# Kernel optimization log

Measured on AMD Instinct MI355X. Metric: run time of the kernel, lower is better.

The kernel has to match this reference:

```python
import jax, jax.numpy as jnp
import numpy as np

B, T, C = 8, 2048, 1024

def setup_inputs() -> dict:
    key = jax.random.key(0)
    ks = jax.random.split(key, 5)
    s_in = 1.0 / np.sqrt(C)
    s3 = 1.0 / np.sqrt(3 * C)
    return {
        'x': jax.random.normal(ks[0], (B, T, C), dtype=jnp.float32),
        'w_attn': jax.random.normal(ks[1], (C, 3 * C), dtype=jnp.float32) * s_in,
        'b_attn': jnp.zeros((3 * C,), dtype=jnp.float32),
        'w_proj': jax.random.normal(ks[2], (C, C), dtype=jnp.float32) * s_in,
        'b_proj': jnp.zeros((C,), dtype=jnp.float32),
    }

def reference(x, w_attn, b_attn, w_proj, b_proj):
    Bv, Tv, Cv = x.shape
    qkv = x @ w_attn + b_attn                      # [B,T,3C]
    q, k, v = jnp.split(qkv, 3, axis=-1)           # each [B,T,C]
    # causal additive mask, matching original -1e10 constant
    mask = jnp.where(jnp.tril(jnp.ones((Tv, Tv), dtype=jnp.bool_)), 0.0, -10000000000.0)
    attn = jnp.einsum('btc,bsc->bts', q, k) / jnp.sqrt(jnp.float32(Cv)) + mask
    attn = jax.nn.softmax(attn, axis=-1)           # [B,T,T]
    out = jnp.einsum('bts,bsc->btc', attn, v)      # [B,T,C]
    return out @ w_proj + b_proj
```

## Files before the change

kernel.cpp:

```cpp
#include <hip/hip_runtime.h>
#include <hip/hip_bf16.h>

typedef __hip_bfloat16 bf16_t;
typedef __attribute__((ext_vector_type(8))) __bf16 bf16x8;
typedef __attribute__((ext_vector_type(4))) float f32x4;
typedef __attribute__((ext_vector_type(8))) unsigned short u16x8;


__device__ __forceinline__ void gld_lds16(const void* g, void* l) {
    __builtin_amdgcn_global_load_lds(
        (const __attribute__((address_space(1))) unsigned int*)g,
        (__attribute__((address_space(3))) unsigned int*)l,
        16, 0, 0);
}

__device__ __forceinline__ unsigned short bf16_bits(float x) {
    bf16_t b = __float2bfloat16(x);
    return *reinterpret_cast<unsigned short*>(&b);
}


__global__ __launch_bounds__(256) void cvt_f32_bf16_kernel(
    const float* __restrict__ in, bf16_t* __restrict__ out, long n4) {
    long stride = (long)gridDim.x * blockDim.x;
    for (long i = (long)blockIdx.x * blockDim.x + threadIdx.x; i < n4; i += stride) {
        float4 v = reinterpret_cast<const float4*>(in)[i];
        ushort4 o;
        o.x = bf16_bits(v.x);
        o.y = bf16_bits(v.y);
        o.z = bf16_bits(v.z);
        o.w = bf16_bits(v.w);
        reinterpret_cast<ushort4*>(out)[i] = o;
    }
}


__global__ __launch_bounds__(256) void transpose_f32_bf16_kernel(
    const float* __restrict__ in, bf16_t* __restrict__ out, long ldin, long ldout) {
    __shared__ float tile[32][33];
    int c0 = blockIdx.x * 32, r0 = blockIdx.y * 32;
    int x = threadIdx.x;
#pragma unroll
    for (int yy = 0; yy < 4; ++yy) {
        int y = threadIdx.y + yy * 8;
        tile[y][x] = in[(long)(r0 + y) * ldin + c0 + x];
    }
    __syncthreads();
#pragma unroll
    for (int yy = 0; yy < 4; ++yy) {
        int y = threadIdx.y + yy * 8;
        out[(long)(c0 + y) * ldout + r0 + x] = __float2bfloat16(tile[x][y]);
    }
}

__global__ __launch_bounds__(256) void transpose_bf16_kernel(
    const bf16_t* __restrict__ in, bf16_t* __restrict__ out,
    long ldin, long ldout, long sIn, long sOut) {
    __shared__ bf16_t tile[32][33];
    in  += (long)blockIdx.z * sIn;
    out += (long)blockIdx.z * sOut;
    int c0 = blockIdx.x * 32, r0 = blockIdx.y * 32;
    int x = threadIdx.x;
#pragma unroll
    for (int yy = 0; yy < 4; ++yy) {
        int y = threadIdx.y + yy * 8;
        tile[y][x] = in[(long)(r0 + y) * ldin + c0 + x];
    }
    __syncthreads();
#pragma unroll
    for (int yy = 0; yy < 4; ++yy) {
        int y = threadIdx.y + yy * 8;
        out[(long)(c0 + y) * ldout + r0 + x] = tile[x][y];
    }
}


__global__ __launch_bounds__(512, 2) void gemm256_kernel(
    const bf16_t* __restrict__ A, const bf16_t* __restrict__ Bt,
    void* __restrict__ Cp, const float* __restrict__ bias,
    float scale, int K,
    long lda, long ldb, long ldc,
    long strideA, long strideB, long strideC,
    int mtiles, int causal_skip, int causal_klimit, int c_f32, int swz_mode)
{
    __shared__ __align__(16) bf16_t As[3][256 * 32];
    __shared__ __align__(16) bf16_t Bs[3][256 * 32];

    int nwg = gridDim.x;
    int bid = blockIdx.x;
    int bm_t, bn_t;
    if (swz_mode == 1 && (mtiles & 7) == 0 && (nwg & 7) == 0) {
        int xcd = bid & 7;
        int l   = bid >> 3;
        int mpx = mtiles >> 3;
        bm_t = xcd * mpx + (l % mpx);
        bn_t = l / mpx;
    } else {
        int swz = (bid & 7) * (nwg >> 3) + (bid >> 3);
        bm_t = swz % mtiles; bn_t = swz / mtiles;
    }
    if (causal_skip && bn_t > bm_t) return;
    long bm0 = (long)bm_t * 256, bn0 = (long)bn_t * 256;

    int b = blockIdx.z;
    const char* Ab = (const char*)(A + (long)b * strideA + bm0 * lda);
    const char* Bb = (const char*)(Bt + (long)b * strideB + bn0 * ldb);
    long ldab = lda * 2, ldbb = ldb * 2;

    int tid = threadIdx.x, wave = tid >> 6, lane = tid & 63;
    int wm = wave >> 2, wn = wave & 3;
    int lr = lane & 15, kc = lane >> 4;

    int Kend = K;
    if (causal_klimit) { long kl = bm0 + 256; Kend = (kl < (long)K) ? (int)kl : K; }
    int NT = Kend >> 5;

    int offw = wave * 1024 + lane * 16;
    int rih  = offw >> 6;
    long colswz = (long)(((lane & 3) ^ ((rih >> 1) & 3)) << 4);
    long rowbA0 = (long)rih * ldab, rowbA1 = (long)(rih + 128) * ldab;
    long rowbB0 = (long)rih * ldbb, rowbB1 = (long)(rih + 128) * ldbb;
    int ldsoff = wave * 1024;

    auto STA = [&](int t, int h, int buf) {
        gld_lds16(Ab + (h ? rowbA1 : rowbA0) + (long)t * 64 + colswz,
                  (char*)As + buf * 16384 + h * 8192 + ldsoff);
    };
    auto STB = [&](int t, int h, int buf) {
        gld_lds16(Bb + (h ? rowbB1 : rowbB0) + (long)t * 64 + colswz,
                  (char*)Bs + buf * 16384 + h * 8192 + ldsoff);
    };

    int aoff[8], boff[4];
#pragma unroll
    for (int m = 0; m < 8; ++m) {
        int row = wm * 128 + m * 16 + lr;
        aoff[m] = (row * 64 + kc * 16) ^ (((row >> 1) & 3) << 4);
    }
#pragma unroll
    for (int n = 0; n < 4; ++n) {
        int row = wn * 64 + n * 16 + lr;
        boff[n] = (row * 64 + kc * 16) ^ (((row >> 1) & 3) << 4);
    }

    f32x4 acc[8][4];
#pragma unroll
    for (int m = 0; m < 8; ++m)
#pragma unroll
        for (int n = 0; n < 4; ++n) acc[m][n] = (f32x4){0.f, 0.f, 0.f, 0.f};

    STA(0, 0, 0); STA(0, 1, 0); STB(0, 0, 0); STB(0, 1, 0);
    STA(1, 0, 1); STA(1, 1, 1); STB(1, 0, 1); STB(1, 1, 1);
    asm volatile("s_waitcnt vmcnt(4)" ::: "memory");
    __builtin_amdgcn_s_barrier();

    int cur = 0;

    for (int t = 0; t < NT; ++t) {
        int b2 = cur + 2; if (b2 >= 3) b2 -= 3;
        int t2 = (t + 2 < NT) ? (t + 2) : NT - 1;
        const char* Ac = (const char*)As + cur * 16384;
        const char* Bc = (const char*)Bs + cur * 16384;

        bf16x8 alo[4], ahi[4], bfr[4];
#pragma unroll
        for (int m = 0; m < 4; ++m) alo[m] = *(const bf16x8*)(Ac + aoff[m]);
#pragma unroll
        for (int n = 0; n < 4; ++n) bfr[n] = *(const bf16x8*)(Bc + boff[n]);
#pragma unroll
        for (int m = 0; m < 4; ++m) ahi[m] = *(const bf16x8*)(Ac + aoff[m + 4]);

        STA(t2, 0, b2); STA(t2, 1, b2);
        STB(t2, 0, b2); STB(t2, 1, b2);
        __builtin_amdgcn_sched_barrier(0);

        __builtin_amdgcn_s_setprio(1);
#pragma unroll
        for (int m = 0; m < 4; ++m)
#pragma unroll
            for (int n = 0; n < 4; ++n)
                acc[m][n] = __builtin_amdgcn_mfma_f32_16x16x32_bf16(alo[m], bfr[n], acc[m][n], 0, 0, 0);
#pragma unroll
        for (int m = 0; m < 4; ++m)
#pragma unroll
            for (int n = 0; n < 4; ++n)
                acc[m + 4][n] = __builtin_amdgcn_mfma_f32_16x16x32_bf16(ahi[m], bfr[n], acc[m + 4][n], 0, 0, 0);
        __builtin_amdgcn_s_setprio(0);

        asm volatile("s_waitcnt vmcnt(4)" ::: "memory");
        __builtin_amdgcn_s_barrier();

        cur += 1; if (cur >= 3) cur -= 3;
    }

    asm volatile("s_waitcnt vmcnt(0)" ::: "memory");

#pragma unroll
    for (int m = 0; m < 8; ++m) {
        long row = bm0 + wm * 128 + m * 16 + kc * 4;
#pragma unroll
        for (int n = 0; n < 4; ++n) {
            long col = bn0 + wn * 64 + n * 16 + lr;
            float bv = bias ? bias[col] : 0.f;
            if (c_f32) {
                float* Crow = (float*)Cp + (long)b * strideC;
#pragma unroll
                for (int r = 0; r < 4; ++r)
                    Crow[(row + r) * ldc + col] = acc[m][n][r] * scale + bv;
            } else {
                bf16_t* Crow = (bf16_t*)Cp + (long)b * strideC;
#pragma unroll
                for (int r = 0; r < 4; ++r)
                    Crow[(row + r) * ldc + col] = __float2bfloat16(acc[m][n][r] * scale + bv);
            }
        }
    }
}


__global__ __launch_bounds__(256) void softmax_causal_kernel(bf16_t* S, int T) {
    int t = blockIdx.x;
    bf16_t* row = S + ((long)blockIdx.y * T + t) * (long)T;
    int tid = threadIdx.x;
    int s0 = tid * 8;
    int klim = ((t >> 8) + 1) << 8;

    u16x8 raw = {};
    if (s0 <= t) raw = *reinterpret_cast<const u16x8*>(&row[s0]);
    float v[8];
#pragma unroll
    for (int j = 0; j < 8; ++j) v[j] = __uint_as_float(((unsigned)raw[j]) << 16);

    float m = -1e30f;
#pragma unroll
    for (int j = 0; j < 8; ++j)
        if (s0 + j <= t) m = fmaxf(m, v[j]);

    __shared__ float red[8];
#pragma unroll
    for (int o = 32; o; o >>= 1) m = fmaxf(m, __shfl_xor(m, o, 64));
    if ((tid & 63) == 0) red[tid >> 6] = m;
    __syncthreads();
    m = fmaxf(fmaxf(red[0], red[1]), fmaxf(red[2], red[3]));
    __syncthreads();

    float e[8];
    float sum = 0.f;
#pragma unroll
    for (int j = 0; j < 8; ++j) {
        e[j] = (s0 + j <= t) ? __expf(v[j] - m) : 0.f;
        sum += e[j];
    }
#pragma unroll
    for (int o = 32; o; o >>= 1) sum += __shfl_xor(sum, o, 64);
    if ((tid & 63) == 0) red[tid >> 6] = sum;
    __syncthreads();
    sum = red[0] + red[1] + red[2] + red[3];
    float inv = 1.f / sum;

    if (s0 < klim) {
        u16x8 outp;
#pragma unroll
        for (int j = 0; j < 8; ++j) outp[j] = bf16_bits(e[j] * inv);
        *reinterpret_cast<u16x8*>(&row[s0]) = outp;
    }
}


extern "C" void kernel_launch(void* const* d_in, const int* in_sizes, int n_in,
                              void* d_out, int out_size, void* d_ws, size_t ws_size,
                              hipStream_t stream) {
    const int B = 8, T = 2048, C = 1024;
    const int M = B * T;
    const int N3 = 3 * C;

    const float* x      = (const float*)d_in[0];
    const float* w_attn = (const float*)d_in[1];
    const float* b_attn = (const float*)d_in[2];
    const float* w_proj = (const float*)d_in[3];
    const float* b_proj = (const float*)d_in[4];
    float* out = (float*)d_out;

    char* ws = (char*)d_ws;

    const size_t BASE_FULL = 142606336ull;
    const size_t PER_B     = 12582912ull;
    long NB = 0;
    if (ws_size >= BASE_FULL + PER_B) {
        NB = (long)((ws_size - BASE_FULL) / PER_B);
        if (NB > 8) NB = 8;
    }

    if (NB >= 1) {
        bf16_t* waT = (bf16_t*)(ws);
        bf16_t* wpT = (bf16_t*)(ws + 6291456);
        bf16_t* qkv = (bf16_t*)(ws + 8388608);
        bf16_t* xbO = (bf16_t*)(ws + 109051904);
        bf16_t* vT  = (bf16_t*)(ws + 142606336);
        bf16_t* S   = (bf16_t*)(ws + 142606336 + (size_t)NB * 4194304);

        cvt_f32_bf16_kernel<<<2048, 256, 0, stream>>>(x, xbO, (long)M * C / 4);

        transpose_f32_bf16_kernel<<<dim3(N3 / 32, C / 32, 1), dim3(32, 8), 0, stream>>>(
            w_attn, waT, N3, C);
        transpose_f32_bf16_kernel<<<dim3(C / 32, C / 32, 1), dim3(32, 8), 0, stream>>>(
            w_proj, wpT, C, C);

        gemm256_kernel<<<dim3((M / 256) * (N3 / 256), 1, 1), 512, 0, stream>>>(
            xbO, waT, qkv, b_attn, 1.0f, C,
            C, C, N3, 0, 0, 0, M / 256, 0, 0, 0, 1);

        for (long b0 = 0; b0 < B; b0 += NB) {
            long nb = (B - b0 < NB) ? (B - b0) : NB;
            const bf16_t* qkv_c = qkv + b0 * (long)T * N3;
            bf16_t* O_c = xbO + b0 * (long)T * C;

            transpose_bf16_kernel<<<dim3(C / 32, T / 32, nb), dim3(32, 8), 0, stream>>>(
                qkv_c + 2 * C, vT, N3, T, (long)T * N3, (long)C * T);

            gemm256_kernel<<<dim3((T / 256) * (T / 256), 1, nb), 512, 0, stream>>>(
                qkv_c, qkv_c + C, S, nullptr, 0.03125f, C,
                N3, N3, T, (long)T * N3, (long)T * N3, (long)T * T, T / 256, 1, 0, 0, 0);

            softmax_causal_kernel<<<dim3(T, nb), 256, 0, stream>>>(S, T);

            gemm256_kernel<<<dim3((T / 256) * (C / 256), 1, nb), 512, 0, stream>>>(
                S, vT, O_c, nullptr, 1.0f, T,
                T, T, C, (long)T * T, (long)C * T, (long)T * C, T / 256, 0, 1, 0, 0);
        }

        gemm256_kernel<<<dim3((M / 256) * (C / 256), 1, 1), 512, 0, stream>>>(
            xbO, wpT, out, b_proj, 1.0f, C,
            C, C, C, 0, 0, 0, M / 256, 0, 0, 1, 1);
    } else {
        bf16_t* waT  = (bf16_t*)(ws);
        bf16_t* wpT  = (bf16_t*)(ws + 6291456);
        bf16_t* xbO  = (bf16_t*)(ws + 8388608);
        bf16_t* qkvb = (bf16_t*)(ws + 12582912);
        bf16_t* vTb  = (bf16_t*)(ws + 25165824);
        bf16_t* Sb   = (bf16_t*)(ws + 29360128);

        transpose_f32_bf16_kernel<<<dim3(N3 / 32, C / 32, 1), dim3(32, 8), 0, stream>>>(
            w_attn, waT, N3, C);
        transpose_f32_bf16_kernel<<<dim3(C / 32, C / 32, 1), dim3(32, 8), 0, stream>>>(
            w_proj, wpT, C, C);

        for (int b = 0; b < B; ++b) {
            const float* x_b = x + (long)b * T * C;
            float* out_b = out + (long)b * T * C;

            cvt_f32_bf16_kernel<<<1024, 256, 0, stream>>>(x_b, xbO, (long)T * C / 4);

            gemm256_kernel<<<dim3((T / 256) * (N3 / 256), 1, 1), 512, 0, stream>>>(
                xbO, waT, qkvb, b_attn, 1.0f, C,
                C, C, N3, 0, 0, 0, T / 256, 0, 0, 0, 1);

            transpose_bf16_kernel<<<dim3(C / 32, T / 32, 1), dim3(32, 8), 0, stream>>>(
                qkvb + 2 * C, vTb, N3, T, 0, 0);

            gemm256_kernel<<<dim3((T / 256) * (T / 256), 1, 1), 512, 0, stream>>>(
                qkvb, qkvb + C, Sb, nullptr, 0.03125f, C,
                N3, N3, T, 0, 0, 0, T / 256, 1, 0, 0, 0);

            softmax_causal_kernel<<<dim3(T, 1), 256, 0, stream>>>(Sb, T);

            gemm256_kernel<<<dim3((T / 256) * (C / 256), 1, 1), 512, 0, stream>>>(
                Sb, vTb, xbO, nullptr, 1.0f, T,
                T, T, C, 0, 0, 0, T / 256, 0, 1, 0, 0);

            gemm256_kernel<<<dim3((T / 256) * (C / 256), 1, 1), 512, 0, stream>>>(
                xbO, wpT, out_b, b_proj, 1.0f, C,
                C, C, C, 0, 0, 0, T / 256, 0, 0, 1, 1);
        }
    }
}
```

Measured before the change: 361.8 us.

## Use four-slot LDS ring and interleave split A/B prefetch with MFMA halves

Grows the GEMM's shared-memory staging ring from three to four slots so slot indices become a cheap bitmask. The K loop is unrolled by two, and each tile's global-to-LDS prefetch is split into an A half and a B half. Each half is issued between the two MFMA sub-blocks, with an extra barrier in the middle, so load issue spreads across the compute. This adds LDS usage and more barriers per tile, and it assumes an even tile count.

```diff
diff --git a/kernel.cpp b/kernel.cpp
--- a/kernel.cpp
+++ b/kernel.cpp
@@ -83,8 +83,8 @@
     long strideA, long strideB, long strideC,
     int mtiles, int causal_skip, int causal_klimit, int c_f32, int swz_mode)
 {
-    __shared__ __align__(16) bf16_t As[3][256 * 32];
-    __shared__ __align__(16) bf16_t Bs[3][256 * 32];
+    __shared__ __align__(16) bf16_t As[4][256 * 32];
+    __shared__ __align__(16) bf16_t Bs[4][256 * 32];
 
     int nwg = gridDim.x;
     int bid = blockIdx.x;
@@ -122,13 +122,13 @@
     long rowbB0 = (long)rih * ldbb, rowbB1 = (long)(rih + 128) * ldbb;
     int ldsoff = wave * 1024;
 
-    auto STA = [&](int t, int h, int buf) {
-        gld_lds16(Ab + (h ? rowbA1 : rowbA0) + (long)t * 64 + colswz,
-                  (char*)As + buf * 16384 + h * 8192 + ldsoff);
+    auto STAGE_A = [&](int t, int slot) {
+        gld_lds16(Ab + rowbA0 + (long)t * 64 + colswz, (char*)As + slot * 16384 + ldsoff);
+        gld_lds16(Ab + rowbA1 + (long)t * 64 + colswz, (char*)As + slot * 16384 + 8192 + ldsoff);
     };
-    auto STB = [&](int t, int h, int buf) {
-        gld_lds16(Bb + (h ? rowbB1 : rowbB0) + (long)t * 64 + colswz,
-                  (char*)Bs + buf * 16384 + h * 8192 + ldsoff);
+    auto STAGE_B = [&](int t, int slot) {
+        gld_lds16(Bb + rowbB0 + (long)t * 64 + colswz, (char*)Bs + slot * 16384 + ldsoff);
+        gld_lds16(Bb + rowbB1 + (long)t * 64 + colswz, (char*)Bs + slot * 16384 + 8192 + ldsoff);
     };
 
     int aoff[8], boff[4];
@@ -149,48 +149,81 @@
 #pragma unroll
         for (int n = 0; n < 4; ++n) acc[m][n] = (f32x4){0.f, 0.f, 0.f, 0.f};
 
-    STA(0, 0, 0); STA(0, 1, 0); STB(0, 0, 0); STB(0, 1, 0);
-    STA(1, 0, 1); STA(1, 1, 1); STB(1, 0, 1); STB(1, 1, 1);
+    STAGE_A(0, 0); STAGE_B(0, 0);
+    STAGE_A(1, 1); STAGE_B(1, 1);
     asm volatile("s_waitcnt vmcnt(4)" ::: "memory");
     __builtin_amdgcn_s_barrier();
 
-    int cur = 0;
-
-    for (int t = 0; t < NT; ++t) {
-        int b2 = cur + 2; if (b2 >= 3) b2 -= 3;
-        int t2 = (t + 2 < NT) ? (t + 2) : NT - 1;
-        const char* Ac = (const char*)As + cur * 16384;
-        const char* Bc = (const char*)Bs + cur * 16384;
-
-        bf16x8 alo[4], ahi[4], bfr[4];
-#pragma unroll
-        for (int m = 0; m < 4; ++m) alo[m] = *(const bf16x8*)(Ac + aoff[m]);
-#pragma unroll
-        for (int n = 0; n < 4; ++n) bfr[n] = *(const bf16x8*)(Bc + boff[n]);
-#pragma unroll
-        for (int m = 0; m < 4; ++m) ahi[m] = *(const bf16x8*)(Ac + aoff[m + 4]);
-
-        STA(t2, 0, b2); STA(t2, 1, b2);
-        STB(t2, 0, b2); STB(t2, 1, b2);
+    int NI = NT >> 1;
+    for (int u = 0; u < NI; ++u) {
+        int e = 2 * u, o = e + 1;
+        int se = e & 3, so = o & 3;
+        int t2 = (e + 2 < NT) ? e + 2 : NT - 1;  int s2 = (e + 2) & 3;
+        int t3 = (o + 2 < NT) ? o + 2 : NT - 1;  int s3 = (o + 2) & 3;
+        const char* AcE = (const char*)As + se * 16384;
+        const char* BcE = (const char*)Bs + se * 16384;
+        const char* AcO = (const char*)As + so * 16384;
+        const char* BcO = (const char*)Bs + so * 16384;
+
+        bf16x8 a0[4], a1[4], bf[4];
+
+#pragma unroll
+        for (int m = 0; m < 4; ++m) a0[m] = *(const bf16x8*)(AcE + aoff[m]);
+#pragma unroll
+        for (int n = 0; n < 4; ++n) bf[n] = *(const bf16x8*)(BcE + boff[n]);
+        STAGE_A(t2, s2);
         __builtin_amdgcn_sched_barrier(0);
-
         __builtin_amdgcn_s_setprio(1);
 #pragma unroll
         for (int m = 0; m < 4; ++m)
 #pragma unroll
             for (int n = 0; n < 4; ++n)
-                acc[m][n] = __builtin_amdgcn_mfma_f32_16x16x32_bf16(alo[m], bfr[n], acc[m][n], 0, 0, 0);
+                acc[m][n] = __builtin_amdgcn_mfma_f32_16x16x32_bf16(a0[m], bf[n], acc[m][n], 0, 0, 0);
+        __builtin_amdgcn_s_setprio(0);
+        __builtin_amdgcn_s_barrier();
+
+#pragma unroll
+        for (int m = 0; m < 4; ++m) a1[m] = *(const bf16x8*)(AcE + aoff[m + 4]);
+        STAGE_B(t2, s2);
+        __builtin_amdgcn_sched_barrier(0);
+        __builtin_amdgcn_s_setprio(1);
 #pragma unroll
         for (int m = 0; m < 4; ++m)
 #pragma unroll
             for (int n = 0; n < 4; ++n)
-                acc[m + 4][n] = __builtin_amdgcn_mfma_f32_16x16x32_bf16(ahi[m], bfr[n], acc[m + 4][n], 0, 0, 0);
+                acc[m + 4][n] = __builtin_amdgcn_mfma_f32_16x16x32_bf16(a1[m], bf[n], acc[m + 4][n], 0, 0, 0);
         __builtin_amdgcn_s_setprio(0);
-
         asm volatile("s_waitcnt vmcnt(4)" ::: "memory");
         __builtin_amdgcn_s_barrier();
 
-        cur += 1; if (cur >= 3) cur -= 3;
+#pragma unroll
+        for (int m = 0; m < 4; ++m) a0[m] = *(const bf16x8*)(AcO + aoff[m]);
+#pragma unroll
+        for (int n = 0; n < 4; ++n) bf[n] = *(const bf16x8*)(BcO + boff[n]);
+        STAGE_A(t3, s3);
+        __builtin_amdgcn_sched_barrier(0);
+        __builtin_amdgcn_s_setprio(1);
+#pragma unroll
+        for (int m = 0; m < 4; ++m)
+#pragma unroll
+            for (int n = 0; n < 4; ++n)
+                acc[m][n] = __builtin_amdgcn_mfma_f32_16x16x32_bf16(a0[m], bf[n], acc[m][n], 0, 0, 0);
+        __builtin_amdgcn_s_setprio(0);
+        __builtin_amdgcn_s_barrier();
+
+#pragma unroll
+        for (int m = 0; m < 4; ++m) a1[m] = *(const bf16x8*)(AcO + aoff[m + 4]);
+        STAGE_B(t3, s3);
+        __builtin_amdgcn_sched_barrier(0);
+        __builtin_amdgcn_s_setprio(1);
+#pragma unroll
+        for (int m = 0; m < 4; ++m)
+#pragma unroll
+            for (int n = 0; n < 4; ++n)
+                acc[m + 4][n] = __builtin_amdgcn_mfma_f32_16x16x32_bf16(a1[m], bf[n], acc[m + 4][n], 0, 0, 0);
+        __builtin_amdgcn_s_setprio(0);
+        asm volatile("s_waitcnt vmcnt(4)" ::: "memory");
+        __builtin_amdgcn_s_barrier();
     }
 
     asm volatile("s_waitcnt vmcnt(0)" ::: "memory");
```

After: 399.1 us. 10.3% more time.
